# Performance work log

Hardware: AMD Instinct MI355X
Metric: run time of the kernel (lower is better)

Reference implementation:

```python
import jax, jax.numpy as jnp
import numpy as np

B, L, D = 2, 2048, 1024
H, HD = 16, 64
MAX_LEN = 4096


def rotate_half(t):
    t1, t2 = jnp.split(t, 2, axis=-1)
    return jnp.concatenate([-t2, t1], axis=-1)


def setup_inputs() -> dict:
    key = jax.random.key(0)
    ks = jax.random.split(key, 6)
    # rope tables computed the standard way (cos/sin of position*inv_freq)
    inv_freq = 1.0 / (10000.0 ** (np.arange(0, HD, 2, dtype=np.float32) / HD))
    pos = np.arange(MAX_LEN, dtype=np.float32)
    freqs = np.einsum('l,f->lf', pos, inv_freq)          # [MAX_LEN, HD/2]
    emb = np.concatenate([freqs, freqs], axis=-1)        # [MAX_LEN, HD]
    return {
        'x': jax.random.normal(ks[0], (B, L, D), dtype=jnp.float32),
        'rope_cos': jnp.asarray(np.cos(emb)),
        'rope_sin': jnp.asarray(np.sin(emb)),
        'W_qkv': jax.random.normal(ks[1], (D, 3 * H * HD), dtype=jnp.float32) * (D ** -0.5),
        'W_out': jax.random.normal(ks[2], (H * HD, D), dtype=jnp.float32) * ((H * HD) ** -0.5),
        'b_out': jnp.zeros((D,), dtype=jnp.float32),
    }


def reference(x, rope_cos, rope_sin, W_qkv, W_out, b_out):
    Bb, Ll, Dd = x.shape
    qkv = jnp.einsum('bld,de->ble', x, W_qkv)            # fused QKV projection
    q, k, v = jnp.split(qkv, 3, axis=-1)
    # [B, h, L, d]
    q = q.reshape(Bb, Ll, H, HD).transpose(0, 2, 1, 3)
    k = k.reshape(Bb, Ll, H, HD).transpose(0, 2, 1, 3)
    v = v.reshape(Bb, Ll, H, HD).transpose(0, 2, 1, 3)
    cos = rope_cos[:Ll][None, None, :, :]                # [1,1,L,d]
    sin = rope_sin[:Ll][None, None, :, :]
    q = q * cos + rotate_half(q) * sin
    k = k * cos + rotate_half(k) * sin
    # causal scaled dot-product attention
    scale = HD ** -0.5
    scores = jnp.einsum('bhqd,bhkd->bhqk', q, k) * scale
    causal = jnp.tril(jnp.ones((Ll, Ll), dtype=bool))
    scores = jnp.where(causal[None, None], scores, jnp.finfo(scores.dtype).min)
    attn = jax.nn.softmax(scores, axis=-1)
    out = jnp.einsum('bhqk,bhkd->bhqd', attn, v)
    out = out.transpose(0, 2, 1, 3).reshape(Bb, Ll, H * HD)
    return jnp.einsum('ble,ed->bld', out, W_out) + b_out
```

## Files before the change

### kernel.cpp

```cpp
#include <hip/hip_runtime.h>
#include <math.h>

#define BQ 2
#define LQ 2048
#define DQ 1024
#define HQ 16
#define HDQ 64

typedef __bf16 bf16_t;
typedef bf16_t bf16x4 __attribute__((ext_vector_type(4)));
typedef bf16_t bf16x8 __attribute__((ext_vector_type(8)));
typedef _Float16 f16_t;
typedef f16_t f16x4 __attribute__((ext_vector_type(4)));
typedef f16_t f16x8 __attribute__((ext_vector_type(8)));
typedef float f32x4 __attribute__((ext_vector_type(4)));

__global__ __launch_bounds__(256) void prep_kernel(
    const float* __restrict__ x, const float* __restrict__ Wqkv,
    const float* __restrict__ Wout, const float* __restrict__ cosT,
    const float* __restrict__ sinT,
    bf16_t* __restrict__ xb, bf16_t* __restrict__ Wqkvt,
    bf16_t* __restrict__ Wot, float4* __restrict__ rpk)
{
    __shared__ float t[32][33];
    const int bid = blockIdx.x, tid = threadIdx.x;
    if (bid < 4096) {
        const int i = (bid * 256 + tid) * 4;
        float4 v = *(const float4*)(x + i);
        bf16x4 o;
        o[0] = (bf16_t)v.x; o[1] = (bf16_t)v.y; o[2] = (bf16_t)v.z; o[3] = (bf16_t)v.w;
        *(bf16x4*)(xb + i) = o;
    } else if (bid < 8192) {
        const bool isq = bid < 7168;
        const int b = isq ? bid - 4096 : bid - 7168;
        const int N = isq ? 3072 : 1024;
        const int gx = isq ? 96 : 32;
        const float* in = isq ? Wqkv : Wout;
        bf16_t* out = isq ? Wqkvt : Wot;
        const int k0 = (b / gx) * 32, n0 = (b % gx) * 32;
        const int r = tid >> 3, c4 = (tid & 7) * 4;
        float4 v = *(const float4*)(in + (size_t)(k0 + r) * N + n0 + c4);
        t[r][c4 + 0] = v.x; t[r][c4 + 1] = v.y;
        t[r][c4 + 2] = v.z; t[r][c4 + 3] = v.w;
        __syncthreads();
        bf16x4 o;
        o[0] = (bf16_t)t[c4 + 0][r]; o[1] = (bf16_t)t[c4 + 1][r];
        o[2] = (bf16_t)t[c4 + 2][r]; o[3] = (bf16_t)t[c4 + 3][r];
        *(bf16x4*)(out + (size_t)(n0 + r) * 1024 + k0 + c4) = o;
    } else {
        const int idx = (bid - 8192) * 256 + tid;
        const int i = idx & 15, l = idx >> 4;
        rpk[idx] = make_float4(cosT[l * 64 + i], cosT[l * 64 + 16 + i],
                               sinT[l * 64 + i], sinT[l * 64 + 16 + i]);
    }
}

__global__ __launch_bounds__(256) void qkv_gemm_kernel(
    const bf16_t* __restrict__ A, const bf16_t* __restrict__ Bt,
    bf16_t* __restrict__ qo, bf16_t* __restrict__ ko, f16_t* __restrict__ vo,
    const float4* __restrict__ rpk)
{
    __shared__ __align__(16) bf16_t As[128][64];
    __shared__ __align__(16) bf16_t Bs[128][64];
    const int K = 1024;
    const int tid  = threadIdx.x;
    const int lane = tid & 63;
    const int w    = tid >> 6;
    const int lr   = lane & 15, quad = lane >> 4;
    const int wm   = w & 1, wn = w >> 1;
    const int m0   = blockIdx.y * 128, n0 = blockIdx.x * 128;
    const int srow8 = lane >> 3;
    const int swz   = ((lane & 7) ^ srow8) * 8;
    const int wc    = (lane & 7) * 8;

    f32x4 acc[4][4];
#pragma unroll
    for (int i = 0; i < 4; i++)
#pragma unroll
        for (int j = 0; j < 4; j++)
#pragma unroll
            for (int r = 0; r < 4; r++) acc[i][j][r] = 0.f;

    bf16x8 ar[4], br[4];
#pragma unroll
    for (int j = 0; j < 4; j++) {
        const int rr = (w * 4 + j) * 8 + srow8;
        ar[j] = *(const bf16x8*)(A  + (size_t)(m0 + rr) * K + swz);
        br[j] = *(const bf16x8*)(Bt + (size_t)(n0 + rr) * K + swz);
    }

    for (int k0 = 0; k0 < K; k0 += 64) {
        __syncthreads();
#pragma unroll
        for (int j = 0; j < 4; j++) {
            const int rg = (w * 4 + j) * 8 + srow8;
            *(bf16x8*)(&As[rg][wc]) = ar[j];
            *(bf16x8*)(&Bs[rg][wc]) = br[j];
        }
        __syncthreads();
        if (k0 + 64 < K) {
#pragma unroll
            for (int j = 0; j < 4; j++) {
                const int rr = (w * 4 + j) * 8 + srow8;
                ar[j] = *(const bf16x8*)(A  + (size_t)(m0 + rr) * K + k0 + 64 + swz);
                br[j] = *(const bf16x8*)(Bt + (size_t)(n0 + rr) * K + k0 + 64 + swz);
            }
        }

        bf16x8 af[4][2], bfr[4][2];
#pragma unroll
        for (int t = 0; t < 4; t++)
#pragma unroll
            for (int h = 0; h < 2; h++) {
                const int cA = ((quad + 4 * h) ^ (lr & 7)) * 8;
                af[t][h]  = *(const bf16x8*)(&As[wm * 64 + t * 16 + lr][cA]);
                bfr[t][h] = *(const bf16x8*)(&Bs[wn * 64 + t * 16 + lr][cA]);
            }
#pragma unroll
        for (int h = 0; h < 2; h++)
#pragma unroll
            for (int mt = 0; mt < 4; mt++)
#pragma unroll
                for (int nt = 0; nt < 4; nt++)
                    acc[mt][nt] = __builtin_amdgcn_mfma_f32_16x16x32_bf16(
                        af[mt][h], bfr[nt][h], acc[mt][nt], 0, 0, 0);
    }

    const int which = n0 >> 10;
    const int h = ((n0 & 1023) + wn * 64) >> 6;
    if (which == 2) {
#pragma unroll
        for (int mt = 0; mt < 4; mt++) {
            const int m = m0 + wm * 64 + mt * 16 + quad * 4;
            const int b = m >> 11, l = m & 2047;
            f16_t* p = vo + ((size_t)(b * HQ + h) * HDQ) * LQ + l;
#pragma unroll
            for (int nt = 0; nt < 4; nt++) {
                f16x4 pv;
#pragma unroll
                for (int r = 0; r < 4; r++) pv[r] = (f16_t)acc[mt][nt][r];
                *(f16x4*)(p + (size_t)(nt * 16 + lr) * LQ) = pv;
            }
        }
    } else {
        bf16_t* dst = which ? ko : qo;
        const float qs = which ? 1.0f : 0.18033688011f;
#pragma unroll
        for (int mt = 0; mt < 4; mt++)
#pragma unroll
            for (int r = 0; r < 4; r++) {
                const int m = m0 + wm * 64 + mt * 16 + quad * 4 + r;
                const int b = m >> 11, l = m & 2047;
                const float4 rp = rpk[l * 16 + lr];
                const float a0 = acc[mt][0][r], a1 = acc[mt][1][r];
                const float a2 = acc[mt][2][r], a3 = acc[mt][3][r];
                bf16_t* p = dst + ((size_t)(b * HQ + h) * LQ + l) * HDQ;
                p[lr]      = (bf16_t)((a0 * rp.x - a2 * rp.z) * qs);
                p[16 + lr] = (bf16_t)((a1 * rp.y - a3 * rp.w) * qs);
                p[32 + lr] = (bf16_t)((a2 * rp.x + a0 * rp.z) * qs);
                p[48 + lr] = (bf16_t)((a3 * rp.y + a1 * rp.w) * qs);
            }
    }
}

__global__ __launch_bounds__(256) void out_gemm_kernel(
    const bf16_t* __restrict__ A, const bf16_t* __restrict__ Bt,
    float* __restrict__ fo, const float* __restrict__ bias)
{
    __shared__ __align__(16) bf16_t As[64][64];
    __shared__ __align__(16) bf16_t Bs[128][64];
    const int K = 1024, N = 1024;
    const int tid  = threadIdx.x;
    const int lane = tid & 63;
    const int w    = tid >> 6;
    const int lr   = lane & 15, quad = lane >> 4;
    const int m0   = blockIdx.y * 64, n0 = blockIdx.x * 128;
    const int srow8 = lane >> 3;
    const int swz   = ((lane & 7) ^ srow8) * 8;
    const int wc    = (lane & 7) * 8;

    f32x4 acc[4][2];
#pragma unroll
    for (int i = 0; i < 4; i++)
#pragma unroll
        for (int j = 0; j < 2; j++)
#pragma unroll
            for (int r = 0; r < 4; r++) acc[i][j][r] = 0.f;

    bf16x8 ar[2], br[4];
#pragma unroll
    for (int j = 0; j < 2; j++)
        ar[j] = *(const bf16x8*)(A + (size_t)(m0 + (w * 2 + j) * 8 + srow8) * K + swz);
#pragma unroll
    for (int j = 0; j < 4; j++)
        br[j] = *(const bf16x8*)(Bt + (size_t)(n0 + (w * 4 + j) * 8 + srow8) * K + swz);

    for (int k0 = 0; k0 < K; k0 += 64) {
        __syncthreads();
#pragma unroll
        for (int j = 0; j < 2; j++)
            *(bf16x8*)(&As[(w * 2 + j) * 8 + srow8][wc]) = ar[j];
#pragma unroll
        for (int j = 0; j < 4; j++)
            *(bf16x8*)(&Bs[(w * 4 + j) * 8 + srow8][wc]) = br[j];
        __syncthreads();
        if (k0 + 64 < K) {
#pragma unroll
            for (int j = 0; j < 2; j++)
                ar[j] = *(const bf16x8*)(A + (size_t)(m0 + (w * 2 + j) * 8 + srow8) * K
                                          + k0 + 64 + swz);
#pragma unroll
            for (int j = 0; j < 4; j++)
                br[j] = *(const bf16x8*)(Bt + (size_t)(n0 + (w * 4 + j) * 8 + srow8) * K
                                          + k0 + 64 + swz);
        }

        bf16x8 af[4][2], bfr[2][2];
#pragma unroll
        for (int h = 0; h < 2; h++) {
            const int cA = ((quad + 4 * h) ^ (lr & 7)) * 8;
#pragma unroll
            for (int t = 0; t < 4; t++)
                af[t][h] = *(const bf16x8*)(&As[t * 16 + lr][cA]);
#pragma unroll
            for (int t = 0; t < 2; t++)
                bfr[t][h] = *(const bf16x8*)(&Bs[w * 32 + t * 16 + lr][cA]);
        }
#pragma unroll
        for (int h = 0; h < 2; h++)
#pragma unroll
            for (int mt = 0; mt < 4; mt++)
#pragma unroll
                for (int nt = 0; nt < 2; nt++)
                    acc[mt][nt] = __builtin_amdgcn_mfma_f32_16x16x32_bf16(
                        af[mt][h], bfr[nt][h], acc[mt][nt], 0, 0, 0);
    }

#pragma unroll
    for (int nt = 0; nt < 2; nt++) {
        const int n = n0 + w * 32 + nt * 16 + lr;
        const float bj = bias[n];
#pragma unroll
        for (int mt = 0; mt < 4; mt++)
#pragma unroll
            for (int r = 0; r < 4; r++) {
                const int m = m0 + mt * 16 + quad * 4 + r;
                fo[(size_t)m * N + n] = acc[mt][nt][r] + bj;
            }
    }
}

__global__ __launch_bounds__(256) void attn_kernel6(
    const bf16_t* __restrict__ qb, const bf16_t* __restrict__ kb,
    const f16_t* __restrict__ vtb, bf16_t* __restrict__ ob)
{
    __shared__ __align__(16) bf16_t Kb[2][64][80];
    __shared__ __align__(16) f16_t  Vs[2][64][72];

    const int tid  = threadIdx.x;
    const int lane = tid & 63;
    const int w    = tid >> 6;
    const int quad = lane >> 4;
    const int lr   = lane & 15;
    const int bh   = blockIdx.x;
    const int qt   = 31 - blockIdx.y;

    const bf16_t* Kh = kb  + (size_t)bh * LQ * HDQ;
    const f16_t*  Vh = vtb + (size_t)bh * HDQ * LQ;

    const int r0 = tid >> 3, c0 = (tid & 7) * 8;
    const int r1 = r0 + 32;

    f16x4 ones;
#pragma unroll
    for (int j = 0; j < 4; j++) ones[j] = (f16_t)1.0f;

    const int qrow = qt * 64 + w * 16 + lr;
    const bf16_t* qp = qb + ((size_t)bh * LQ + qrow) * HDQ;
    const bf16x8 qa0 = *(const bf16x8*)(qp + quad * 8);
    const bf16x8 qa1 = *(const bf16x8*)(qp + 32 + quad * 8);

    bf16x8 kp0 = *(const bf16x8*)(Kh + (size_t)r0 * HDQ + c0);
    bf16x8 kp1 = *(const bf16x8*)(Kh + (size_t)r1 * HDQ + c0);
    f16x8  vp0 = *(const f16x8*)(Vh + (size_t)r0 * LQ + c0);
    f16x8  vp1 = *(const f16x8*)(Vh + (size_t)r1 * LQ + c0);

    f32x4 Oacc[4], lacc;
#pragma unroll
    for (int d = 0; d < 4; d++)
#pragma unroll
        for (int r = 0; r < 4; r++) Oacc[d][r] = 0.f;
#pragma unroll
    for (int r = 0; r < 4; r++) lacc[r] = 0.f;

    for (int kt = 0; kt <= qt; kt++) {
        const int buf = kt & 1;
        *(bf16x8*)(&Kb[buf][r0][c0]) = kp0;
        *(bf16x8*)(&Kb[buf][r1][c0]) = kp1;
        *(f16x8*)(&Vs[buf][r0][c0]) = vp0;
        *(f16x8*)(&Vs[buf][r1][c0]) = vp1;
        __syncthreads();
        if (kt < qt) {
            const bf16_t* kn = Kh + (size_t)(kt + 1) * 64 * HDQ;
            kp0 = *(const bf16x8*)(kn + (size_t)r0 * HDQ + c0);
            kp1 = *(const bf16x8*)(kn + (size_t)r1 * HDQ + c0);
            vp0 = *(const f16x8*)(Vh + (size_t)r0 * LQ + (kt + 1) * 64 + c0);
            vp1 = *(const f16x8*)(Vh + (size_t)r1 * LQ + (kt + 1) * 64 + c0);
        }

        f32x4 s[4];
#pragma unroll
        for (int nt = 0; nt < 4; nt++) {
            const bf16x8 kf0 = *(const bf16x8*)(&Kb[buf][nt * 16 + lr][quad * 8]);
            const bf16x8 kf1 = *(const bf16x8*)(&Kb[buf][nt * 16 + lr][32 + quad * 8]);
            f32x4 z = {0.f, 0.f, 0.f, 0.f};
            z = __builtin_amdgcn_mfma_f32_16x16x32_bf16(kf0, qa0, z, 0, 0, 0);
            z = __builtin_amdgcn_mfma_f32_16x16x32_bf16(kf1, qa1, z, 0, 0, 0);
            s[nt] = z;
        }
        if (kt == qt) {
#pragma unroll
            for (int nt = 0; nt < 4; nt++)
#pragma unroll
                for (int r = 0; r < 4; r++)
                    if (nt * 16 + quad * 4 + r > w * 16 + lr) s[nt][r] = -INFINITY;
        }
        f16x4 pa[4];
#pragma unroll
        for (int nt = 0; nt < 4; nt++)
#pragma unroll
            for (int r = 0; r < 4; r++)
                pa[nt][r] = (f16_t)__builtin_amdgcn_exp2f(s[nt][r]);

#pragma unroll
        for (int d = 0; d < 4; d++)
#pragma unroll
            for (int nt = 0; nt < 4; nt++) {
                const f16x4 vf = *(const f16x4*)(&Vs[buf][d * 16 + lr][nt * 16 + quad * 4]);
                Oacc[d] = __builtin_amdgcn_mfma_f32_16x16x16f16(pa[nt], vf, Oacc[d], 0, 0, 0);
            }
#pragma unroll
        for (int nt = 0; nt < 4; nt++)
            lacc = __builtin_amdgcn_mfma_f32_16x16x16f16(pa[nt], ones, lacc, 0, 0, 0);
    }

    const int b = bh >> 4, h = bh & 15;
#pragma unroll
    for (int r = 0; r < 4; r++) {
        const float inv = 1.0f / lacc[r];
        const int q = qt * 64 + w * 16 + quad * 4 + r;
        bf16_t* op = ob + ((size_t)(b * LQ + q)) * 1024 + h * 64;
#pragma unroll
        for (int d = 0; d < 4; d++)
            op[d * 16 + lr] = (bf16_t)(Oacc[d][r] * inv);
    }
}

extern "C" void kernel_launch(void* const* d_in, const int* in_sizes, int n_in,
                              void* d_out, int out_size, void* d_ws, size_t ws_size,
                              hipStream_t stream) {
    const float* x        = (const float*)d_in[0];
    const float* rope_cos = (const float*)d_in[1];
    const float* rope_sin = (const float*)d_in[2];
    const float* W_qkv    = (const float*)d_in[3];
    const float* W_out    = (const float*)d_in[4];
    const float* b_out    = (const float*)d_in[5];
    float* out = (float*)d_out;

    char* wsb = (char*)d_ws;
    bf16_t* xb    = (bf16_t*)(wsb);
    bf16_t* qbf   = (bf16_t*)(wsb + ((size_t)8  << 20));
    bf16_t* kbf   = (bf16_t*)(wsb + ((size_t)16 << 20));
    f16_t*  vth   = (f16_t*) (wsb + ((size_t)24 << 20));
    bf16_t* ob    = (bf16_t*)(wsb + ((size_t)32 << 20));
    bf16_t* Wqkvt = (bf16_t*)(wsb + ((size_t)40 << 20));
    bf16_t* Wot   = (bf16_t*)(wsb + ((size_t)46 << 20));
    float4* rpk   = (float4*)(wsb + ((size_t)48 << 20));

    prep_kernel<<<8320, 256, 0, stream>>>(x, W_qkv, W_out, rope_cos, rope_sin,
                                          xb, Wqkvt, Wot, rpk);

    dim3 g1(3072 / 128, 4096 / 128);
    qkv_gemm_kernel<<<g1, 256, 0, stream>>>(xb, Wqkvt, qbf, kbf, vth, rpk);

    dim3 g2(32, 32);
    attn_kernel6<<<g2, 256, 0, stream>>>(qbf, kbf, vth, ob);

    dim3 g3(1024 / 128, 4096 / 64);
    out_gemm_kernel<<<g3, 256, 0, stream>>>(ob, Wot, out, b_out);
}
```

Before: 173.2 us.

## Use direct global-to-LDS loads in GEMMs and raise priority around attention MFMAs

```diff
diff --git a/kernel.cpp b/kernel.cpp
--- a/kernel.cpp
+++ b/kernel.cpp
@@ -14,6 +14,12 @@
 typedef f16_t f16x4 __attribute__((ext_vector_type(4)));
 typedef f16_t f16x8 __attribute__((ext_vector_type(8)));
 typedef float f32x4 __attribute__((ext_vector_type(4)));
+
+__device__ __forceinline__ void gl2lds16(const bf16_t* g, bf16_t* l) {
+    __builtin_amdgcn_global_load_lds(
+        (const __attribute__((address_space(1))) unsigned int*)g,
+        (__attribute__((address_space(3))) unsigned int*)l, 16, 0, 0);
+}
 
 __global__ __launch_bounds__(256) void prep_kernel(
     const float* __restrict__ x, const float* __restrict__ Wqkv,
@@ -71,7 +77,6 @@
     const int m0   = blockIdx.y * 128, n0 = blockIdx.x * 128;
     const int srow8 = lane >> 3;
     const int swz   = ((lane & 7) ^ srow8) * 8;
-    const int wc    = (lane & 7) * 8;
 
     f32x4 acc[4][4];
 #pragma unroll
@@ -81,31 +86,15 @@
 #pragma unroll
             for (int r = 0; r < 4; r++) acc[i][j][r] = 0.f;
 
-    bf16x8 ar[4], br[4];
-#pragma unroll
-    for (int j = 0; j < 4; j++) {
-        const int rr = (w * 4 + j) * 8 + srow8;
-        ar[j] = *(const bf16x8*)(A  + (size_t)(m0 + rr) * K + swz);
-        br[j] = *(const bf16x8*)(Bt + (size_t)(n0 + rr) * K + swz);
-    }
-
     for (int k0 = 0; k0 < K; k0 += 64) {
         __syncthreads();
 #pragma unroll
         for (int j = 0; j < 4; j++) {
-            const int rg = (w * 4 + j) * 8 + srow8;
-            *(bf16x8*)(&As[rg][wc]) = ar[j];
-            *(bf16x8*)(&Bs[rg][wc]) = br[j];
-        }
-        __syncthreads();
-        if (k0 + 64 < K) {
-#pragma unroll
-            for (int j = 0; j < 4; j++) {
-                const int rr = (w * 4 + j) * 8 + srow8;
-                ar[j] = *(const bf16x8*)(A  + (size_t)(m0 + rr) * K + k0 + 64 + swz);
-                br[j] = *(const bf16x8*)(Bt + (size_t)(n0 + rr) * K + k0 + 64 + swz);
-            }
-        }
+            const int rg = (w * 4 + j) * 8;
+            gl2lds16(A  + (size_t)(m0 + rg + srow8) * K + k0 + swz, &As[rg][0]);
+            gl2lds16(Bt + (size_t)(n0 + rg + srow8) * K + k0 + swz, &Bs[rg][0]);
+        }
+        __syncthreads();
 
         bf16x8 af[4][2], bfr[4][2];
 #pragma unroll
@@ -177,7 +166,6 @@
     const int m0   = blockIdx.y * 64, n0 = blockIdx.x * 128;
     const int srow8 = lane >> 3;
     const int swz   = ((lane & 7) ^ srow8) * 8;
-    const int wc    = (lane & 7) * 8;
 
     f32x4 acc[4][2];
 #pragma unroll
@@ -187,33 +175,19 @@
 #pragma unroll
             for (int r = 0; r < 4; r++) acc[i][j][r] = 0.f;
 
-    bf16x8 ar[2], br[4];
-#pragma unroll
-    for (int j = 0; j < 2; j++)
-        ar[j] = *(const bf16x8*)(A + (size_t)(m0 + (w * 2 + j) * 8 + srow8) * K + swz);
-#pragma unroll
-    for (int j = 0; j < 4; j++)
-        br[j] = *(const bf16x8*)(Bt + (size_t)(n0 + (w * 4 + j) * 8 + srow8) * K + swz);
-
     for (int k0 = 0; k0 < K; k0 += 64) {
         __syncthreads();
 #pragma unroll
-        for (int j = 0; j < 2; j++)
-            *(bf16x8*)(&As[(w * 2 + j) * 8 + srow8][wc]) = ar[j];
-#pragma unroll
-        for (int j = 0; j < 4; j++)
-            *(bf16x8*)(&Bs[(w * 4 + j) * 8 + srow8][wc]) = br[j];
-        __syncthreads();
-        if (k0 + 64 < K) {
-#pragma unroll
-            for (int j = 0; j < 2; j++)
-                ar[j] = *(const bf16x8*)(A + (size_t)(m0 + (w * 2 + j) * 8 + srow8) * K
-                                          + k0 + 64 + swz);
-#pragma unroll
-            for (int j = 0; j < 4; j++)
-                br[j] = *(const bf16x8*)(Bt + (size_t)(n0 + (w * 4 + j) * 8 + srow8) * K
-                                          + k0 + 64 + swz);
-        }
+        for (int j = 0; j < 2; j++) {
+            const int rg = (w * 2 + j) * 8;
+            gl2lds16(A + (size_t)(m0 + rg + srow8) * K + k0 + swz, &As[rg][0]);
+        }
+#pragma unroll
+        for (int j = 0; j < 4; j++) {
+            const int rg = (w * 4 + j) * 8;
+            gl2lds16(Bt + (size_t)(n0 + rg + srow8) * K + k0 + swz, &Bs[rg][0]);
+        }
+        __syncthreads();
 
         bf16x8 af[4][2], bfr[2][2];
 #pragma unroll
@@ -309,6 +283,7 @@
         }
 
         f32x4 s[4];
+        __builtin_amdgcn_s_setprio(1);
 #pragma unroll
         for (int nt = 0; nt < 4; nt++) {
             const bf16x8 kf0 = *(const bf16x8*)(&Kb[buf][nt * 16 + lr][quad * 8]);
@@ -318,6 +293,7 @@
             z = __builtin_amdgcn_mfma_f32_16x16x32_bf16(kf1, qa1, z, 0, 0, 0);
             s[nt] = z;
         }
+        __builtin_amdgcn_s_setprio(0);
         if (kt == qt) {
 #pragma unroll
             for (int nt = 0; nt < 4; nt++)
@@ -332,6 +308,7 @@
             for (int r = 0; r < 4; r++)
                 pa[nt][r] = (f16_t)__builtin_amdgcn_exp2f(s[nt][r]);
 
+        __builtin_amdgcn_s_setprio(1);
 #pragma unroll
         for (int d = 0; d < 4; d++)
 #pragma unroll
@@ -342,6 +319,7 @@
 #pragma unroll
         for (int nt = 0; nt < 4; nt++)
             lacc = __builtin_amdgcn_mfma_f32_16x16x16f16(pa[nt], ones, lacc, 0, 0, 0);
+        __builtin_amdgcn_s_setprio(0);
     }
 
     const int b = bh >> 4, h = bh & 15;
```

After: 183.5 us. 5.9% more time.
